# Kernel tuning notes

Measured on AMD Instinct MI355X. Metric: run time of the kernel, lower is better.

The kernel has to match this reference:

```python
import jax, jax.numpy as jnp
import numpy as np

N_QUBITS = 4
INV_SQRT2 = 0.7071067811865476
B, D_IN, D_OUT, N_LAYERS = 32768, 2048, 2048, 2


def _apply_1q(state, gate, w):
    # state: [B,2,2,2,2]; gate: [2,2] or [B,2,2]; acts on wire w (axis w+1)
    s = jnp.moveaxis(state, w + 1, 1)
    if gate.ndim == 3:
        s = jnp.einsum('bij,bjklm->biklm', gate, s)
    else:
        s = jnp.einsum('ij,bjklm->biklm', gate, s)
    return jnp.moveaxis(s, 1, w + 1)


def _apply_cnot(state, c, t):
    # control wire c, target wire t: flip target bit on the control=1 slice
    s0 = jnp.take(state, 0, axis=c + 1)
    s1 = jnp.take(state, 1, axis=c + 1)
    t_ax = t + 1 - (1 if t > c else 0)  # target axis after removing control axis
    s1 = jnp.flip(s1, axis=t_ax)
    return jnp.stack([s0, s1], axis=c + 1)


def _ry(theta):  # [B] -> [B,2,2]
    c = jnp.cos(theta / 2)
    s = jnp.sin(theta / 2)
    m = jnp.stack([jnp.stack([c, -s], -1), jnp.stack([s, c], -1)], -2)
    return m.astype(jnp.complex64)


def _rz(theta):  # [B] -> [B,2,2] diag(e^{-i t/2}, e^{i t/2})
    e = jnp.exp(-0.5j * theta.astype(jnp.complex64))
    z = jnp.zeros_like(e)
    return jnp.stack([jnp.stack([e, z], -1), jnp.stack([z, jnp.conj(e)], -1)], -2)


def _rot(phi, theta, omega):  # PennyLane Rot = RZ(omega) @ RY(theta) @ RZ(phi)
    c = jnp.cos(theta / 2)
    s = jnp.sin(theta / 2)
    ep = jnp.exp(-0.5j * (phi + omega).astype(jnp.complex64))
    em = jnp.exp(0.5j * (phi - omega).astype(jnp.complex64))
    return jnp.stack([jnp.stack([ep * c, -em * s]),
                      jnp.stack([jnp.conj(em) * s, jnp.conj(ep) * c])])


def _circuit(a, q_weights):
    # a: [B,4] angles; q_weights: [L,4,3]; returns [B,4] PauliZ expvals
    b = a.shape[0]
    state = jnp.zeros((b, 16), jnp.complex64).at[:, 0].set(1.0).reshape(b, 2, 2, 2, 2)
    H = jnp.array([[1.0, 1.0], [1.0, -1.0]], jnp.complex64) * INV_SQRT2
    for i in range(N_QUBITS):
        f = a[:, i]
        state = _apply_1q(state, H, i)
        state = _apply_1q(state, _ry(jnp.arctan(f)), i)
        state = _apply_1q(state, _rz(jnp.arctan(f * f)), i)
    for l in range(q_weights.shape[0]):
        for i in range(N_QUBITS):
            state = _apply_cnot(state, i, (i + 1) % N_QUBITS)
        for i in range(N_QUBITS):
            g = _rot(q_weights[l, i, 0], q_weights[l, i, 1], q_weights[l, i, 2])
            state = _apply_1q(state, g, i)
    probs = jnp.abs(state) ** 2
    zs = []
    for w in range(N_QUBITS):
        axes = tuple(ax for ax in range(1, 5) if ax != w + 1)
        m = probs.sum(axis=axes)  # [B,2] marginal of wire w
        zs.append(m[:, 0] - m[:, 1])
    return jnp.stack(zs, axis=-1)


def setup_inputs() -> dict:
    key = jax.random.key(0)
    ks = jax.random.split(key, 6)
    return {
        'x': jax.random.normal(ks[0], (B, D_IN), jnp.float32),
        'W_pre': jax.random.normal(ks[1], (N_QUBITS, D_IN), jnp.float32) * (1.0 / np.sqrt(D_IN)),
        'b_pre': jax.random.normal(ks[2], (N_QUBITS,), jnp.float32) * 0.01,
        'q_weights': jax.random.normal(ks[3], (N_LAYERS, N_QUBITS, 3), jnp.float32),
        'W_post': jax.random.normal(ks[4], (D_OUT, N_QUBITS), jnp.float32) * 0.5,
        'b_post': jax.random.normal(ks[5], (D_OUT,), jnp.float32) * 0.01,
    }


def reference(x, W_pre, b_pre, q_weights, W_post, b_post):
    a = jnp.tanh(x @ W_pre.T + b_pre) * jnp.pi      # [B,4]
    q = _circuit(a, q_weights)                       # [B,4] real expvals
    return q @ W_post.T + b_post                     # [B,D_OUT]
```

## Files before the change

kernel.cpp:

```cpp
#include <hip/hip_runtime.h>
#include <cmath>


namespace {

constexpr int   kB        = 32768;
constexpr int   kDin      = 2048;
constexpr int   kDout     = 2048;
constexpr int   kRows     = 8;
constexpr float kPi       = 3.14159265358979323846f;
constexpr float kInvSqrt2 = 0.70710678118654752440f;

__device__ __forceinline__ float2 cmul(float2 a, float2 b) {
    return make_float2(a.x * b.x - a.y * b.y, a.x * b.y + a.y * b.x);
}

__global__ __launch_bounds__(256) void qproj_kernel(
    const float* __restrict__ x,
    const float* __restrict__ W_pre,
    const float* __restrict__ b_pre,
    const float* __restrict__ qw,
    const float* __restrict__ W_post,
    const float* __restrict__ b_post,
    float* __restrict__ out)
{
    const int lane    = threadIdx.x & 63;
    const int wv      = threadIdx.x >> 6;
    const int wave_id = (blockIdx.x << 2) + wv;
    const int row0    = wave_id * kRows;

    float my_s[4] = {0.f, 0.f, 0.f, 0.f};
#pragma unroll 1
    for (int r = 0; r < kRows; ++r) {
        const float* xrow = x + (size_t)(row0 + r) * kDin;
        float acc[4] = {0.f, 0.f, 0.f, 0.f};
#pragma unroll
        for (int it = 0; it < kDin / 256; ++it) {
            const int k = it * 256 + lane * 4;
            const float4 xv = *(const float4*)(xrow + k);
            const float4 w0 = *(const float4*)(W_pre + 0 * kDin + k);
            const float4 w1 = *(const float4*)(W_pre + 1 * kDin + k);
            const float4 w2 = *(const float4*)(W_pre + 2 * kDin + k);
            const float4 w3 = *(const float4*)(W_pre + 3 * kDin + k);
            acc[0] += xv.x * w0.x + xv.y * w0.y + xv.z * w0.z + xv.w * w0.w;
            acc[1] += xv.x * w1.x + xv.y * w1.y + xv.z * w1.z + xv.w * w1.w;
            acc[2] += xv.x * w2.x + xv.y * w2.y + xv.z * w2.z + xv.w * w2.w;
            acc[3] += xv.x * w3.x + xv.y * w3.y + xv.z * w3.z + xv.w * w3.w;
        }
#pragma unroll
        for (int off = 32; off > 0; off >>= 1) {
#pragma unroll
            for (int i = 0; i < 4; ++i) acc[i] += __shfl_xor(acc[i], off);
        }
        if (lane == r) {
#pragma unroll
            for (int i = 0; i < 4; ++i) my_s[i] = acc[i];
        }
    }

    float av[4];
#pragma unroll
    for (int i = 0; i < 4; ++i) av[i] = tanhf(my_s[i] + b_pre[i]) * kPi;

    float2 st[16];
#pragma unroll
    for (int i = 0; i < 16; ++i) st[i] = make_float2(0.f, 0.f);
    st[0] = make_float2(1.f, 0.f);

#pragma unroll
    for (int q = 0; q < 4; ++q) {
        const int bq = 1 << q;
        const float f = av[q];
        float sr, cr;  sincosf(0.5f * atanf(f),     &sr, &cr);
        float sz, cz;  sincosf(0.5f * atanf(f * f), &sz, &cz);
        const float u = kInvSqrt2 * (cr - sr);
        const float v = kInvSqrt2 * (cr + sr);
        const float2 e  = make_float2(cz, -sz);
        const float2 ec = make_float2(cz,  sz);
#pragma unroll
        for (int idx = 0; idx < 16; ++idx) {
            if (idx & bq) continue;
            const float2 a0 = st[idx], a1 = st[idx | bq];
            const float2 t0 = make_float2(u * a0.x + v * a1.x, u * a0.y + v * a1.y);
            const float2 t1 = make_float2(v * a0.x - u * a1.x, v * a0.y - u * a1.y);
            st[idx]      = cmul(e,  t0);
            st[idx | bq] = cmul(ec, t1);
        }
    }

#pragma unroll
    for (int l = 0; l < 2; ++l) {
#pragma unroll
        for (int c = 0; c < 4; ++c) {
            const int t  = (c + 1) & 3;
            const int bc = 1 << c, bt = 1 << t;
#pragma unroll
            for (int idx = 0; idx < 16; ++idx) {
                if ((idx & bc) && !(idx & bt)) {
                    const float2 tmp = st[idx];
                    st[idx]      = st[idx | bt];
                    st[idx | bt] = tmp;
                }
            }
        }
#pragma unroll
        for (int q = 0; q < 4; ++q) {
            const int bq = 1 << q;
            const float phi = qw[l * 12 + q * 3 + 0];
            const float th  = qw[l * 12 + q * 3 + 1];
            const float om  = qw[l * 12 + q * 3 + 2];
            float s2, c2;  sincosf(0.5f * th,         &s2, &c2);
            float sp, cp;  sincosf(0.5f * (phi + om), &sp, &cp);
            float sm, cm;  sincosf(0.5f * (phi - om), &sm, &cm);
            const float2 m00 = make_float2( cp * c2, -sp * c2);
            const float2 m01 = make_float2(-cm * s2, -sm * s2);
            const float2 m10 = make_float2( cm * s2, -sm * s2);
            const float2 m11 = make_float2( cp * c2,  sp * c2);
#pragma unroll
            for (int idx = 0; idx < 16; ++idx) {
                if (idx & bq) continue;
                const float2 a0 = st[idx], a1 = st[idx | bq];
                float2 n0 = cmul(m00, a0), u01 = cmul(m01, a1);
                n0.x += u01.x; n0.y += u01.y;
                float2 n1 = cmul(m10, a0), u11 = cmul(m11, a1);
                n1.x += u11.x; n1.y += u11.y;
                st[idx]      = n0;
                st[idx | bq] = n1;
            }
        }
    }

    float z[4] = {0.f, 0.f, 0.f, 0.f};
#pragma unroll
    for (int idx = 0; idx < 16; ++idx) {
        const float p = st[idx].x * st[idx].x + st[idx].y * st[idx].y;
#pragma unroll
        for (int w = 0; w < 4; ++w) z[w] += (idx & (1 << w)) ? -p : p;
    }

    float zb[kRows][4];
#pragma unroll
    for (int r = 0; r < kRows; ++r) {
#pragma unroll
        for (int c = 0; c < 4; ++c) zb[r][c] = __shfl(z[c], r);
    }

    float* obase = out + (size_t)row0 * kDout;
#pragma unroll 1
    for (int it = 0; it < kDout / 256; ++it) {
        const int j = it * 256 + lane * 4;
        const float4 bp = *(const float4*)(b_post + j);
        const float4 wa = *(const float4*)(W_post + (size_t)(j + 0) * 4);
        const float4 wb = *(const float4*)(W_post + (size_t)(j + 1) * 4);
        const float4 wc = *(const float4*)(W_post + (size_t)(j + 2) * 4);
        const float4 wd = *(const float4*)(W_post + (size_t)(j + 3) * 4);
#pragma unroll
        for (int r = 0; r < kRows; ++r) {
            float4 o;
            o.x = zb[r][0] * wa.x + zb[r][1] * wa.y + zb[r][2] * wa.z + zb[r][3] * wa.w + bp.x;
            o.y = zb[r][0] * wb.x + zb[r][1] * wb.y + zb[r][2] * wb.z + zb[r][3] * wb.w + bp.y;
            o.z = zb[r][0] * wc.x + zb[r][1] * wc.y + zb[r][2] * wc.z + zb[r][3] * wc.w + bp.z;
            o.w = zb[r][0] * wd.x + zb[r][1] * wd.y + zb[r][2] * wd.z + zb[r][3] * wd.w + bp.w;
            *(float4*)(obase + (size_t)r * kDout + j) = o;
        }
    }
}

}

extern "C" void kernel_launch(void* const* d_in, const int* in_sizes, int n_in,
                              void* d_out, int out_size, void* d_ws, size_t ws_size,
                              hipStream_t stream) {
    const float* x      = (const float*)d_in[0];
    const float* W_pre  = (const float*)d_in[1];
    const float* b_pre  = (const float*)d_in[2];
    const float* qw     = (const float*)d_in[3];
    const float* W_post = (const float*)d_in[4];
    const float* b_post = (const float*)d_in[5];
    float* out = (float*)d_out;

    qproj_kernel<<<dim3(kB / (4 * kRows)), dim3(256), 0, stream>>>(
        x, W_pre, b_pre, qw, W_post, b_post, out);
}
```

Before: 500.2 us.

## Split fused kernel into dots, circuit, and post-projection kernels via workspace

Splits the single fused kernel into three launches. The first computes the x·W_pre dot products four rows per wave with interleaved loads, the second simulates the 4-qubit circuit with one row per thread, and the third runs the output projection as a wide, coalesced streaming store. All three pass intermediates through the workspace. The aim is to stop the circuit simulation from idling 56 of 64 lanes and to give the read-bound and write-bound phases their own launch shapes. The cost is two extra launches and a small workspace round trip, and the old fused kernel is kept as a fallback when no workspace is provided.

```diff
diff --git a/kernel.cpp b/kernel.cpp
--- a/kernel.cpp
+++ b/kernel.cpp
@@ -7,7 +7,6 @@
 constexpr int   kB        = 32768;
 constexpr int   kDin      = 2048;
 constexpr int   kDout     = 2048;
-constexpr int   kRows     = 8;
 constexpr float kPi       = 3.14159265358979323846f;
 constexpr float kInvSqrt2 = 0.70710678118654752440f;
 
@@ -15,52 +14,63 @@
     return make_float2(a.x * b.x - a.y * b.y, a.x * b.y + a.y * b.x);
 }
 
-__global__ __launch_bounds__(256) void qproj_kernel(
+__global__ __launch_bounds__(256) void dots_kernel(
     const float* __restrict__ x,
     const float* __restrict__ W_pre,
+    float*       __restrict__ s_out)
+{
+    const int lane = threadIdx.x & 63;
+    const int wv   = threadIdx.x >> 6;
+    const int row0 = ((blockIdx.x << 2) + wv) << 2;
+
+    float acc[4][4];
+#pragma unroll
+    for (int r = 0; r < 4; ++r)
+#pragma unroll
+        for (int c = 0; c < 4; ++c) acc[r][c] = 0.f;
+
+#pragma unroll
+    for (int it = 0; it < kDin / 256; ++it) {
+        const int k = it * 256 + lane * 4;
+        const float4 w0 = *(const float4*)(W_pre + 0 * kDin + k);
+        const float4 w1 = *(const float4*)(W_pre + 1 * kDin + k);
+        const float4 w2 = *(const float4*)(W_pre + 2 * kDin + k);
+        const float4 w3 = *(const float4*)(W_pre + 3 * kDin + k);
+#pragma unroll
+        for (int r = 0; r < 4; ++r) {
+            const float4 xv = *(const float4*)(x + (size_t)(row0 + r) * kDin + k);
+            acc[r][0] += xv.x * w0.x + xv.y * w0.y + xv.z * w0.z + xv.w * w0.w;
+            acc[r][1] += xv.x * w1.x + xv.y * w1.y + xv.z * w1.z + xv.w * w1.w;
+            acc[r][2] += xv.x * w2.x + xv.y * w2.y + xv.z * w2.z + xv.w * w2.w;
+            acc[r][3] += xv.x * w3.x + xv.y * w3.y + xv.z * w3.z + xv.w * w3.w;
+        }
+    }
+
+#pragma unroll
+    for (int off = 32; off > 0; off >>= 1) {
+#pragma unroll
+        for (int r = 0; r < 4; ++r)
+#pragma unroll
+            for (int c = 0; c < 4; ++c) acc[r][c] += __shfl_xor(acc[r][c], off);
+    }
+
+    if (lane < 4) {
+        *(float4*)(s_out + (size_t)(row0 + lane) * 4) =
+            make_float4(acc[lane][0], acc[lane][1], acc[lane][2], acc[lane][3]);
+    }
+}
+
+__global__ __launch_bounds__(256) void circuit_kernel(
+    float*       __restrict__ sz,
     const float* __restrict__ b_pre,
-    const float* __restrict__ qw,
-    const float* __restrict__ W_post,
-    const float* __restrict__ b_post,
-    float* __restrict__ out)
+    const float* __restrict__ qw)
 {
-    const int lane    = threadIdx.x & 63;
-    const int wv      = threadIdx.x >> 6;
-    const int wave_id = (blockIdx.x << 2) + wv;
-    const int row0    = wave_id * kRows;
-
-    float my_s[4] = {0.f, 0.f, 0.f, 0.f};
-#pragma unroll 1
-    for (int r = 0; r < kRows; ++r) {
-        const float* xrow = x + (size_t)(row0 + r) * kDin;
-        float acc[4] = {0.f, 0.f, 0.f, 0.f};
-#pragma unroll
-        for (int it = 0; it < kDin / 256; ++it) {
-            const int k = it * 256 + lane * 4;
-            const float4 xv = *(const float4*)(xrow + k);
-            const float4 w0 = *(const float4*)(W_pre + 0 * kDin + k);
-            const float4 w1 = *(const float4*)(W_pre + 1 * kDin + k);
-            const float4 w2 = *(const float4*)(W_pre + 2 * kDin + k);
-            const float4 w3 = *(const float4*)(W_pre + 3 * kDin + k);
-            acc[0] += xv.x * w0.x + xv.y * w0.y + xv.z * w0.z + xv.w * w0.w;
-            acc[1] += xv.x * w1.x + xv.y * w1.y + xv.z * w1.z + xv.w * w1.w;
-            acc[2] += xv.x * w2.x + xv.y * w2.y + xv.z * w2.z + xv.w * w2.w;
-            acc[3] += xv.x * w3.x + xv.y * w3.y + xv.z * w3.z + xv.w * w3.w;
-        }
-#pragma unroll
-        for (int off = 32; off > 0; off >>= 1) {
-#pragma unroll
-            for (int i = 0; i < 4; ++i) acc[i] += __shfl_xor(acc[i], off);
-        }
-        if (lane == r) {
-#pragma unroll
-            for (int i = 0; i < 4; ++i) my_s[i] = acc[i];
-        }
-    }
-
-    float av[4];
-#pragma unroll
-    for (int i = 0; i < 4; ++i) av[i] = tanhf(my_s[i] + b_pre[i]) * kPi;
+    const int row = blockIdx.x * 256 + threadIdx.x;
+    const float4 sv = *(const float4*)(sz + (size_t)row * 4);
+    float av[4] = { tanhf(sv.x + b_pre[0]) * kPi,
+                    tanhf(sv.y + b_pre[1]) * kPi,
+                    tanhf(sv.z + b_pre[2]) * kPi,
+                    tanhf(sv.w + b_pre[3]) * kPi };
 
     float2 st[16];
 #pragma unroll
@@ -72,11 +82,11 @@
         const int bq = 1 << q;
         const float f = av[q];
         float sr, cr;  sincosf(0.5f * atanf(f),     &sr, &cr);
-        float sz, cz;  sincosf(0.5f * atanf(f * f), &sz, &cz);
+        float sz_, cz; sincosf(0.5f * atanf(f * f), &sz_, &cz);
         const float u = kInvSqrt2 * (cr - sr);
         const float v = kInvSqrt2 * (cr + sr);
-        const float2 e  = make_float2(cz, -sz);
-        const float2 ec = make_float2(cz,  sz);
+        const float2 e  = make_float2(cz, -sz_);
+        const float2 ec = make_float2(cz,  sz_);
 #pragma unroll
         for (int idx = 0; idx < 16; ++idx) {
             if (idx & bq) continue;
@@ -137,13 +147,158 @@
 #pragma unroll
         for (int w = 0; w < 4; ++w) z[w] += (idx & (1 << w)) ? -p : p;
     }
-
-    float zb[kRows][4];
-#pragma unroll
-    for (int r = 0; r < kRows; ++r) {
+    *(float4*)(sz + (size_t)row * 4) = make_float4(z[0], z[1], z[2], z[3]);
+}
+
+__global__ __launch_bounds__(256) void post_kernel(
+    const float* __restrict__ z,
+    const float* __restrict__ W_post,
+    const float* __restrict__ b_post,
+    float*       __restrict__ out)
+{
+    const int tid  = threadIdx.x;
+    const int jt   = blockIdx.x & 1;
+    const int rb   = blockIdx.x >> 1;
+    const int j    = jt * 1024 + tid * 4;
+    const int row0 = rb * 32;
+
+    const float4 wa = *(const float4*)(W_post + (size_t)j * 4);
+    const float4 wb = *(const float4*)(W_post + (size_t)j * 4 + 4);
+    const float4 wc = *(const float4*)(W_post + (size_t)j * 4 + 8);
+    const float4 wd = *(const float4*)(W_post + (size_t)j * 4 + 12);
+    const float4 bp = *(const float4*)(b_post + j);
+
+    float* obase = out + (size_t)row0 * kDout + j;
+#pragma unroll 8
+    for (int r = 0; r < 32; ++r) {
+        const float4 zv = *(const float4*)(z + (size_t)(row0 + r) * 4);
+        float4 o;
+        o.x = zv.x * wa.x + zv.y * wa.y + zv.z * wa.z + zv.w * wa.w + bp.x;
+        o.y = zv.x * wb.x + zv.y * wb.y + zv.z * wb.z + zv.w * wb.w + bp.y;
+        o.z = zv.x * wc.x + zv.y * wc.y + zv.z * wc.z + zv.w * wc.w + bp.z;
+        o.w = zv.x * wd.x + zv.y * wd.y + zv.z * wd.z + zv.w * wd.w + bp.w;
+        *(float4*)(obase + (size_t)r * kDout) = o;
+    }
+}
+
+__global__ __launch_bounds__(256) void qproj_fused(
+    const float* __restrict__ x, const float* __restrict__ W_pre,
+    const float* __restrict__ b_pre, const float* __restrict__ qw,
+    const float* __restrict__ W_post, const float* __restrict__ b_post,
+    float* __restrict__ out)
+{
+    const int lane = threadIdx.x & 63;
+    const int wv   = threadIdx.x >> 6;
+    const int row0 = ((blockIdx.x << 2) + wv) * 8;
+
+    float my_s[4] = {0.f, 0.f, 0.f, 0.f};
+#pragma unroll 1
+    for (int r = 0; r < 8; ++r) {
+        const float* xrow = x + (size_t)(row0 + r) * kDin;
+        float acc[4] = {0.f, 0.f, 0.f, 0.f};
+#pragma unroll
+        for (int it = 0; it < kDin / 256; ++it) {
+            const int k = it * 256 + lane * 4;
+            const float4 xv = *(const float4*)(xrow + k);
+            const float4 w0 = *(const float4*)(W_pre + 0 * kDin + k);
+            const float4 w1 = *(const float4*)(W_pre + 1 * kDin + k);
+            const float4 w2 = *(const float4*)(W_pre + 2 * kDin + k);
+            const float4 w3 = *(const float4*)(W_pre + 3 * kDin + k);
+            acc[0] += xv.x * w0.x + xv.y * w0.y + xv.z * w0.z + xv.w * w0.w;
+            acc[1] += xv.x * w1.x + xv.y * w1.y + xv.z * w1.z + xv.w * w1.w;
+            acc[2] += xv.x * w2.x + xv.y * w2.y + xv.z * w2.z + xv.w * w2.w;
+            acc[3] += xv.x * w3.x + xv.y * w3.y + xv.z * w3.z + xv.w * w3.w;
+        }
+#pragma unroll
+        for (int off = 32; off > 0; off >>= 1)
+#pragma unroll
+            for (int i = 0; i < 4; ++i) acc[i] += __shfl_xor(acc[i], off);
+        if (lane == r)
+#pragma unroll
+            for (int i = 0; i < 4; ++i) my_s[i] = acc[i];
+    }
+
+    float av[4];
+#pragma unroll
+    for (int i = 0; i < 4; ++i) av[i] = tanhf(my_s[i] + b_pre[i]) * kPi;
+
+    float2 st[16];
+#pragma unroll
+    for (int i = 0; i < 16; ++i) st[i] = make_float2(0.f, 0.f);
+    st[0] = make_float2(1.f, 0.f);
+#pragma unroll
+    for (int q = 0; q < 4; ++q) {
+        const int bq = 1 << q;
+        const float f = av[q];
+        float sr, cr;  sincosf(0.5f * atanf(f),     &sr, &cr);
+        float sz, cz;  sincosf(0.5f * atanf(f * f), &sz, &cz);
+        const float u = kInvSqrt2 * (cr - sr);
+        const float v = kInvSqrt2 * (cr + sr);
+        const float2 e  = make_float2(cz, -sz);
+        const float2 ec = make_float2(cz,  sz);
+#pragma unroll
+        for (int idx = 0; idx < 16; ++idx) {
+            if (idx & bq) continue;
+            const float2 a0 = st[idx], a1 = st[idx | bq];
+            const float2 t0 = make_float2(u * a0.x + v * a1.x, u * a0.y + v * a1.y);
+            const float2 t1 = make_float2(v * a0.x - u * a1.x, v * a0.y - u * a1.y);
+            st[idx]      = cmul(e,  t0);
+            st[idx | bq] = cmul(ec, t1);
+        }
+    }
+#pragma unroll
+    for (int l = 0; l < 2; ++l) {
+#pragma unroll
+        for (int c = 0; c < 4; ++c) {
+            const int t  = (c + 1) & 3;
+            const int bc = 1 << c, bt = 1 << t;
+#pragma unroll
+            for (int idx = 0; idx < 16; ++idx) {
+                if ((idx & bc) && !(idx & bt)) {
+                    const float2 tmp = st[idx];
+                    st[idx]      = st[idx | bt];
+                    st[idx | bt] = tmp;
+                }
+            }
+        }
+#pragma unroll
+        for (int q = 0; q < 4; ++q) {
+            const int bq = 1 << q;
+            const float phi = qw[l * 12 + q * 3 + 0];
+            const float th  = qw[l * 12 + q * 3 + 1];
+            const float om  = qw[l * 12 + q * 3 + 2];
+            float s2, c2;  sincosf(0.5f * th,         &s2, &c2);
+            float sp, cp;  sincosf(0.5f * (phi + om), &sp, &cp);
+            float sm, cm;  sincosf(0.5f * (phi - om), &sm, &cm);
+            const float2 m00 = make_float2( cp * c2, -sp * c2);
+            const float2 m01 = make_float2(-cm * s2, -sm * s2);
+            const float2 m10 = make_float2( cm * s2, -sm * s2);
+            const float2 m11 = make_float2( cp * c2,  sp * c2);
+#pragma unroll
+            for (int idx = 0; idx < 16; ++idx) {
+                if (idx & bq) continue;
+                const float2 a0 = st[idx], a1 = st[idx | bq];
+                float2 n0 = cmul(m00, a0), u01 = cmul(m01, a1);
+                n0.x += u01.x; n0.y += u01.y;
+                float2 n1 = cmul(m10, a0), u11 = cmul(m11, a1);
+                n1.x += u11.x; n1.y += u11.y;
+                st[idx]      = n0;
+                st[idx | bq] = n1;
+            }
+        }
+    }
+    float z[4] = {0.f, 0.f, 0.f, 0.f};
+#pragma unroll
+    for (int idx = 0; idx < 16; ++idx) {
+        const float p = st[idx].x * st[idx].x + st[idx].y * st[idx].y;
+#pragma unroll
+        for (int w = 0; w < 4; ++w) z[w] += (idx & (1 << w)) ? -p : p;
+    }
+    float zb[8][4];
+#pragma unroll
+    for (int r = 0; r < 8; ++r)
 #pragma unroll
         for (int c = 0; c < 4; ++c) zb[r][c] = __shfl(z[c], r);
-    }
 
     float* obase = out + (size_t)row0 * kDout;
 #pragma unroll 1
@@ -155,7 +310,7 @@
         const float4 wc = *(const float4*)(W_post + (size_t)(j + 2) * 4);
         const float4 wd = *(const float4*)(W_post + (size_t)(j + 3) * 4);
 #pragma unroll
-        for (int r = 0; r < kRows; ++r) {
+        for (int r = 0; r < 8; ++r) {
             float4 o;
             o.x = zb[r][0] * wa.x + zb[r][1] * wa.y + zb[r][2] * wa.z + zb[r][3] * wa.w + bp.x;
             o.y = zb[r][0] * wb.x + zb[r][1] * wb.y + zb[r][2] * wb.z + zb[r][3] * wb.w + bp.y;
@@ -179,6 +334,14 @@
     const float* b_post = (const float*)d_in[5];
     float* out = (float*)d_out;
 
-    qproj_kernel<<<dim3(kB / (4 * kRows)), dim3(256), 0, stream>>>(
-        x, W_pre, b_pre, qw, W_post, b_post, out);
-}
+    const size_t z_bytes = (size_t)kB * 4 * sizeof(float);
+    if (d_ws != nullptr && ws_size >= z_bytes) {
+        float* sz = (float*)d_ws;
+        dots_kernel<<<dim3(kB / 16), dim3(256), 0, stream>>>(x, W_pre, sz);
+        circuit_kernel<<<dim3(kB / 256), dim3(256), 0, stream>>>(sz, b_pre, qw);
+        post_kernel<<<dim3(2 * (kB / 32)), dim3(256), 0, stream>>>(sz, W_post, b_post, out);
+    } else {
+        qproj_fused<<<dim3(kB / 32), dim3(256), 0, stream>>>(
+            x, W_pre, b_pre, qw, W_post, b_post, out);
+    }
+}
```

After: 501.2 us. No clear change (+0.2%).

## Split into dot+circuit kernel and streaming output-projection kernel via workspace

Applied to the files above, without the earlier changes.

Splits the fused kernel into two. The first does the input projection and quantum circuit, with all 8 rows' loads in flight per iteration instead of looping row by row, and writes the 4-value results to a workspace. The second reads those and streams the 2048-wide output using nontemporal vector stores with shared-memory broadcast of z. The aim is more memory-level parallelism on the 256MB read and 256MB write phases. The cost is an extra launch, a small intermediate buffer, and more registers for 32 accumulators. The old fused kernel remains as a fallback when no workspace is available.

```diff
diff --git a/kernel.cpp b/kernel.cpp
--- a/kernel.cpp
+++ b/kernel.cpp
@@ -7,61 +7,18 @@
 constexpr int   kB        = 32768;
 constexpr int   kDin      = 2048;
 constexpr int   kDout     = 2048;
-constexpr int   kRows     = 8;
 constexpr float kPi       = 3.14159265358979323846f;
 constexpr float kInvSqrt2 = 0.70710678118654752440f;
 
+typedef float vfloat4 __attribute__((ext_vector_type(4)));
+
 __device__ __forceinline__ float2 cmul(float2 a, float2 b) {
     return make_float2(a.x * b.x - a.y * b.y, a.x * b.y + a.y * b.x);
 }
 
-__global__ __launch_bounds__(256) void qproj_kernel(
-    const float* __restrict__ x,
-    const float* __restrict__ W_pre,
-    const float* __restrict__ b_pre,
-    const float* __restrict__ qw,
-    const float* __restrict__ W_post,
-    const float* __restrict__ b_post,
-    float* __restrict__ out)
-{
-    const int lane    = threadIdx.x & 63;
-    const int wv      = threadIdx.x >> 6;
-    const int wave_id = (blockIdx.x << 2) + wv;
-    const int row0    = wave_id * kRows;
-
-    float my_s[4] = {0.f, 0.f, 0.f, 0.f};
-#pragma unroll 1
-    for (int r = 0; r < kRows; ++r) {
-        const float* xrow = x + (size_t)(row0 + r) * kDin;
-        float acc[4] = {0.f, 0.f, 0.f, 0.f};
-#pragma unroll
-        for (int it = 0; it < kDin / 256; ++it) {
-            const int k = it * 256 + lane * 4;
-            const float4 xv = *(const float4*)(xrow + k);
-            const float4 w0 = *(const float4*)(W_pre + 0 * kDin + k);
-            const float4 w1 = *(const float4*)(W_pre + 1 * kDin + k);
-            const float4 w2 = *(const float4*)(W_pre + 2 * kDin + k);
-            const float4 w3 = *(const float4*)(W_pre + 3 * kDin + k);
-            acc[0] += xv.x * w0.x + xv.y * w0.y + xv.z * w0.z + xv.w * w0.w;
-            acc[1] += xv.x * w1.x + xv.y * w1.y + xv.z * w1.z + xv.w * w1.w;
-            acc[2] += xv.x * w2.x + xv.y * w2.y + xv.z * w2.z + xv.w * w2.w;
-            acc[3] += xv.x * w3.x + xv.y * w3.y + xv.z * w3.z + xv.w * w3.w;
-        }
-#pragma unroll
-        for (int off = 32; off > 0; off >>= 1) {
-#pragma unroll
-            for (int i = 0; i < 4; ++i) acc[i] += __shfl_xor(acc[i], off);
-        }
-        if (lane == r) {
-#pragma unroll
-            for (int i = 0; i < 4; ++i) my_s[i] = acc[i];
-        }
-    }
-
-    float av[4];
-#pragma unroll
-    for (int i = 0; i < 4; ++i) av[i] = tanhf(my_s[i] + b_pre[i]) * kPi;
-
+__device__ __forceinline__ void run_circuit(const float av[4],
+                                            const float* __restrict__ qw,
+                                            float z[4]) {
     float2 st[16];
 #pragma unroll
     for (int i = 0; i < 16; ++i) st[i] = make_float2(0.f, 0.f);
@@ -72,11 +29,11 @@
         const int bq = 1 << q;
         const float f = av[q];
         float sr, cr;  sincosf(0.5f * atanf(f),     &sr, &cr);
-        float sz, cz;  sincosf(0.5f * atanf(f * f), &sz, &cz);
+        float sz_, cz; sincosf(0.5f * atanf(f * f), &sz_, &cz);
         const float u = kInvSqrt2 * (cr - sr);
         const float v = kInvSqrt2 * (cr + sr);
-        const float2 e  = make_float2(cz, -sz);
-        const float2 ec = make_float2(cz,  sz);
+        const float2 e  = make_float2(cz, -sz_);
+        const float2 ec = make_float2(cz,  sz_);
 #pragma unroll
         for (int idx = 0; idx < 16; ++idx) {
             if (idx & bq) continue;
@@ -130,20 +87,163 @@
         }
     }
 
-    float z[4] = {0.f, 0.f, 0.f, 0.f};
+    z[0] = z[1] = z[2] = z[3] = 0.f;
 #pragma unroll
     for (int idx = 0; idx < 16; ++idx) {
         const float p = st[idx].x * st[idx].x + st[idx].y * st[idx].y;
 #pragma unroll
         for (int w = 0; w < 4; ++w) z[w] += (idx & (1 << w)) ? -p : p;
     }
-
-    float zb[kRows][4];
-#pragma unroll
-    for (int r = 0; r < kRows; ++r) {
+}
+
+__global__ __launch_bounds__(256) void dots_circuit_kernel(
+    const float* __restrict__ x,
+    const float* __restrict__ W_pre,
+    const float* __restrict__ b_pre,
+    const float* __restrict__ qw,
+    float*       __restrict__ z_out)
+{
+    const int lane = threadIdx.x & 63;
+    const int wv   = threadIdx.x >> 6;
+    const int row0 = (((blockIdx.x << 2) + wv) << 3);
+
+    float acc[8][4];
+#pragma unroll
+    for (int r = 0; r < 8; ++r)
+#pragma unroll
+        for (int c = 0; c < 4; ++c) acc[r][c] = 0.f;
+
+#pragma unroll 2
+    for (int it = 0; it < kDin / 256; ++it) {
+        const int k = it * 256 + lane * 4;
+        const float4 w0 = *(const float4*)(W_pre + 0 * kDin + k);
+        const float4 w1 = *(const float4*)(W_pre + 1 * kDin + k);
+        const float4 w2 = *(const float4*)(W_pre + 2 * kDin + k);
+        const float4 w3 = *(const float4*)(W_pre + 3 * kDin + k);
+#pragma unroll
+        for (int r = 0; r < 8; ++r) {
+            const float4 xv = *(const float4*)(x + (size_t)(row0 + r) * kDin + k);
+            acc[r][0] += xv.x * w0.x + xv.y * w0.y + xv.z * w0.z + xv.w * w0.w;
+            acc[r][1] += xv.x * w1.x + xv.y * w1.y + xv.z * w1.z + xv.w * w1.w;
+            acc[r][2] += xv.x * w2.x + xv.y * w2.y + xv.z * w2.z + xv.w * w2.w;
+            acc[r][3] += xv.x * w3.x + xv.y * w3.y + xv.z * w3.z + xv.w * w3.w;
+        }
+    }
+
+#pragma unroll
+    for (int off = 32; off > 0; off >>= 1) {
+#pragma unroll
+        for (int r = 0; r < 8; ++r)
+#pragma unroll
+            for (int c = 0; c < 4; ++c) acc[r][c] += __shfl_xor(acc[r][c], off);
+    }
+
+    float my_s[4] = {0.f, 0.f, 0.f, 0.f};
+#pragma unroll
+    for (int rr = 0; rr < 8; ++rr) {
+        if (lane == rr) {
+#pragma unroll
+            for (int c = 0; c < 4; ++c) my_s[c] = acc[rr][c];
+        }
+    }
+
+    float av[4];
+#pragma unroll
+    for (int c = 0; c < 4; ++c) av[c] = tanhf(my_s[c] + b_pre[c]) * kPi;
+
+    float z[4];
+    run_circuit(av, qw, z);
+
+    if (lane < 8) {
+        *(float4*)(z_out + (size_t)(row0 + lane) * 4) =
+            make_float4(z[0], z[1], z[2], z[3]);
+    }
+}
+
+__global__ __launch_bounds__(256) void post_kernel(
+    const float* __restrict__ z,
+    const float* __restrict__ W_post,
+    const float* __restrict__ b_post,
+    float*       __restrict__ out)
+{
+    const int tid  = threadIdx.x;
+    const int jt   = blockIdx.x & 1;
+    const int rb   = blockIdx.x >> 1;
+    const int j    = jt * 1024 + tid * 4;
+    const int row0 = rb * 32;
+
+    __shared__ float4 zsh[32];
+
+    const float4 wa = *(const float4*)(W_post + (size_t)j * 4);
+    const float4 wb = *(const float4*)(W_post + (size_t)j * 4 + 4);
+    const float4 wc = *(const float4*)(W_post + (size_t)j * 4 + 8);
+    const float4 wd = *(const float4*)(W_post + (size_t)j * 4 + 12);
+    const float4 bp = *(const float4*)(b_post + j);
+
+    if (tid < 32) zsh[tid] = *(const float4*)(z + (size_t)(row0 + tid) * 4);
+    __syncthreads();
+
+    float* obase = out + (size_t)row0 * kDout + j;
+#pragma unroll
+    for (int r = 0; r < 32; ++r) {
+        const float4 zv = zsh[r];
+        vfloat4 o;
+        o.x = zv.x * wa.x + zv.y * wa.y + zv.z * wa.z + zv.w * wa.w + bp.x;
+        o.y = zv.x * wb.x + zv.y * wb.y + zv.z * wb.z + zv.w * wb.w + bp.y;
+        o.z = zv.x * wc.x + zv.y * wc.y + zv.z * wc.z + zv.w * wc.w + bp.z;
+        o.w = zv.x * wd.x + zv.y * wd.y + zv.z * wd.z + zv.w * wd.w + bp.w;
+        __builtin_nontemporal_store(o, (vfloat4*)(obase + (size_t)r * kDout));
+    }
+}
+
+__global__ __launch_bounds__(256) void qproj_fused(
+    const float* __restrict__ x, const float* __restrict__ W_pre,
+    const float* __restrict__ b_pre, const float* __restrict__ qw,
+    const float* __restrict__ W_post, const float* __restrict__ b_post,
+    float* __restrict__ out)
+{
+    const int lane = threadIdx.x & 63;
+    const int wv   = threadIdx.x >> 6;
+    const int row0 = ((blockIdx.x << 2) + wv) * 8;
+
+    float my_s[4] = {0.f, 0.f, 0.f, 0.f};
+#pragma unroll 1
+    for (int r = 0; r < 8; ++r) {
+        const float* xrow = x + (size_t)(row0 + r) * kDin;
+        float acc[4] = {0.f, 0.f, 0.f, 0.f};
+#pragma unroll
+        for (int it = 0; it < kDin / 256; ++it) {
+            const int k = it * 256 + lane * 4;
+            const float4 xv = *(const float4*)(xrow + k);
+            const float4 w0 = *(const float4*)(W_pre + 0 * kDin + k);
+            const float4 w1 = *(const float4*)(W_pre + 1 * kDin + k);
+            const float4 w2 = *(const float4*)(W_pre + 2 * kDin + k);
+            const float4 w3 = *(const float4*)(W_pre + 3 * kDin + k);
+            acc[0] += xv.x * w0.x + xv.y * w0.y + xv.z * w0.z + xv.w * w0.w;
+            acc[1] += xv.x * w1.x + xv.y * w1.y + xv.z * w1.z + xv.w * w1.w;
+            acc[2] += xv.x * w2.x + xv.y * w2.y + xv.z * w2.z + xv.w * w2.w;
+            acc[3] += xv.x * w3.x + xv.y * w3.y + xv.z * w3.z + xv.w * w3.w;
+        }
+#pragma unroll
+        for (int off = 32; off > 0; off >>= 1)
+#pragma unroll
+            for (int i = 0; i < 4; ++i) acc[i] += __shfl_xor(acc[i], off);
+        if (lane == r)
+#pragma unroll
+            for (int i = 0; i < 4; ++i) my_s[i] = acc[i];
+    }
+
+    float av[4];
+#pragma unroll
+    for (int i = 0; i < 4; ++i) av[i] = tanhf(my_s[i] + b_pre[i]) * kPi;
+    float z[4];
+    run_circuit(av, qw, z);
+
+    float zb[8][4];
+#pragma unroll
+    for (int r = 0; r < 8; ++r)
 #pragma unroll
         for (int c = 0; c < 4; ++c) zb[r][c] = __shfl(z[c], r);
-    }
 
     float* obase = out + (size_t)row0 * kDout;
 #pragma unroll 1
@@ -155,7 +255,7 @@
         const float4 wc = *(const float4*)(W_post + (size_t)(j + 2) * 4);
         const float4 wd = *(const float4*)(W_post + (size_t)(j + 3) * 4);
 #pragma unroll
-        for (int r = 0; r < kRows; ++r) {
+        for (int r = 0; r < 8; ++r) {
             float4 o;
             o.x = zb[r][0] * wa.x + zb[r][1] * wa.y + zb[r][2] * wa.z + zb[r][3] * wa.w + bp.x;
             o.y = zb[r][0] * wb.x + zb[r][1] * wb.y + zb[r][2] * wb.z + zb[r][3] * wb.w + bp.y;
@@ -179,6 +279,15 @@
     const float* b_post = (const float*)d_in[5];
     float* out = (float*)d_out;
 
-    qproj_kernel<<<dim3(kB / (4 * kRows)), dim3(256), 0, stream>>>(
-        x, W_pre, b_pre, qw, W_post, b_post, out);
-}
+    const size_t z_bytes = (size_t)kB * 4 * sizeof(float);
+    if (d_ws != nullptr && ws_size >= z_bytes) {
+        float* zbuf = (float*)d_ws;
+        dots_circuit_kernel<<<dim3(kB / 32), dim3(256), 0, stream>>>(
+            x, W_pre, b_pre, qw, zbuf);
+        post_kernel<<<dim3(2 * (kB / 32)), dim3(256), 0, stream>>>(
+            zbuf, W_post, b_post, out);
+    } else {
+        qproj_fused<<<dim3(kB / 32), dim3(256), 0, stream>>>(
+            x, W_pre, b_pre, qw, W_post, b_post, out);
+    }
+}
```

After: 467.0 us. 6.6% less time.
